# Optimization experiments

Hardware: AMD Instinct MI355X
Metric: run time of the kernel (lower is better)

The kernel has to match this reference:

```python
import jax, jax.numpy as jnp
import numpy as np

B, H, W, C, NH = 400, 14, 14, 768, 12
HD = C // NH  # 64


def setup_inputs() -> dict:
    key = jax.random.key(0)
    ks = jax.random.split(key, 6)
    s = 0.02
    return {
        "hidden_states": jax.random.normal(ks[0], (B, H, W, C), jnp.float32),
        "qkv_w": jax.random.normal(ks[1], (3 * C, C), jnp.float32) * s,
        "qkv_b": jnp.zeros((3 * C,), jnp.float32),
        "proj_w": jax.random.normal(ks[2], (C, C), jnp.float32) * s,
        "proj_b": jnp.zeros((C,), jnp.float32),
        "rel_pos_h": jax.random.normal(ks[3], (2 * H - 1, HD), jnp.float32) * s,
        "rel_pos_w": jax.random.normal(ks[4], (2 * W - 1, HD), jnp.float32) * s,
    }


def _get_rel_pos(q_size, k_size, rel_pos):
    # q_size == k_size and table already has 2*k-1 entries -> pure gather,
    # matching SamVisionAttention.get_rel_pos without interpolation.
    coords = jnp.arange(q_size)[:, None] - jnp.arange(k_size)[None, :] + (k_size - 1)
    return rel_pos[coords]  # (q, k, head_dim)


def reference(hidden_states, qkv_w, qkv_b, proj_w, proj_b, rel_pos_h, rel_pos_w):
    b, h, w, c = hidden_states.shape
    scale = HD ** -0.5
    # qkv projection: (b, h*w, 3c) -> (3, b, nh, hw, hd)
    qkv = hidden_states.reshape(b, h * w, c) @ qkv_w.T + qkv_b
    qkv = qkv.reshape(b, h * w, 3, NH, HD).transpose(2, 0, 3, 1, 4)
    q, k, v = qkv[0], qkv[1], qkv[2]
    # decomposed relative position bias (computed from UNSCALED q, as in SAM)
    Rh = _get_rel_pos(h, h, rel_pos_h)  # (h, h, hd)
    Rw = _get_rel_pos(w, w, rel_pos_w)  # (w, w, hd)
    qr = q.reshape(b, NH, h, w, HD)
    rel_h = jnp.einsum('bnhwc,hkc->bnhwk', qr, Rh)  # (b, nh, h, w, h)
    rel_w = jnp.einsum('bnhwc,wkc->bnhwk', qr, Rw)  # (b, nh, h, w, w)
    bias = (rel_h[..., :, None] + rel_w[..., None, :]).reshape(b, NH, h * w, h * w)
    # attention
    attn = jnp.einsum('bnqd,bnkd->bnqk', q, k) * scale + bias
    attn = jax.nn.softmax(attn, axis=-1)
    out = jnp.einsum('bnqk,bnkd->bnqd', attn, v)
    out = out.transpose(0, 2, 1, 3).reshape(b, h, w, c)
    return out @ proj_w.T + proj_b
```

## Files before the change

kernel.cpp:

```cpp
#include <hip/hip_runtime.h>
#include <hip/hip_bf16.h>

typedef __bf16 bfv8 __attribute__((ext_vector_type(8)));
typedef float f32x4 __attribute__((ext_vector_type(4)));
typedef unsigned short u16;
typedef unsigned int u32;

#define MT 78400

#define SBAR() __builtin_amdgcn_s_barrier()
#define VMCNT(n) asm volatile("s_waitcnt vmcnt(" #n ")" ::: "memory")

__device__ __forceinline__ u16 f2bf(float f) {
  u32 x = __float_as_uint(f);
  return (u16)((x + 0x7FFFu + ((x >> 16) & 1u)) >> 16);
}

__device__ __forceinline__ void gld16(const void* g, void* l) {
  __builtin_amdgcn_global_load_lds((const __attribute__((address_space(1))) void*)g,
                                   (__attribute__((address_space(3))) void*)l, 16, 0, 0);
}

__global__ __launch_bounds__(256) void cvt_f32_bf16(const float* __restrict__ src,
                                                    u16* __restrict__ dst, int n8) {
  int stride = gridDim.x * 256;
  for (int i = blockIdx.x * 256 + threadIdx.x; i < n8; i += stride) {
    const float4* s = (const float4*)(src + (long)i * 8);
    float4 a = s[0], b = s[1];
    u32 p0 = f2bf(a.x) | ((u32)f2bf(a.y) << 16);
    u32 p1 = f2bf(a.z) | ((u32)f2bf(a.w) << 16);
    u32 p2 = f2bf(b.x) | ((u32)f2bf(b.y) << 16);
    u32 p3 = f2bf(b.z) | ((u32)f2bf(b.w) << 16);
    uint4 o = {p0, p1, p2, p3};
    *(uint4*)(dst + (long)i * 8) = o;
  }
}


__device__ __forceinline__ void gemm256_main(const u16* __restrict__ A, const u16* __restrict__ W,
                                             u16* SH, int m0, int n0, int tid,
                                             f32x4 (&acc)[8][4]) {
  const int lane = tid & 63;
  const int q15 = lane & 15, g = lane >> 4;
  const int wid = tid >> 6;
  const int wm = wid >> 2, wn = wid & 3;
  const int x0 = (g ^ (q15 & 7)) << 3;
  const int arow0 = wm * 128 + q15;
  const int brow0 = wn * 64 + q15;

  const int r0 = tid >> 3;
  const int gc0 = ((tid & 7) ^ (r0 & 7)) << 3;
  int ra00 = m0 + r0;       if (ra00 > MT - 1) ra00 = MT - 1;
  int ra10 = m0 + 64 + r0;  if (ra10 > MT - 1) ra10 = MT - 1;
  int ra01 = m0 + 128 + r0; if (ra01 > MT - 1) ra01 = MT - 1;
  int ra11 = m0 + 192 + r0; if (ra11 > MT - 1) ra11 = MT - 1;
  const u16* aS00 = A + (long)ra00 * 768 + gc0;
  const u16* aS10 = A + (long)ra10 * 768 + gc0;
  const u16* aS01 = A + (long)ra01 * 768 + gc0;
  const u16* aS11 = A + (long)ra11 * 768 + gc0;
  const u16* bS00 = W + (long)(n0 + r0) * 768 + gc0;
  const u16* bS10 = W + (long)(n0 + 64 + r0) * 768 + gc0;
  const u16* bS01 = W + (long)(n0 + 128 + r0) * 768 + gc0;
  const u16* bS11 = W + (long)(n0 + 192 + r0) * 768 + gc0;
  u16* dA = SH + tid * 8;
  u16* dB = dA + 16384;

  auto STGA = [&](int sl, const u16* p0, const u16* p1, int hoff, int kt) {
    u16* d = dA + sl * 32768 + hoff;
    gld16(p0 + kt * 64, d);
    gld16(p1 + kt * 64, d + 4096);
  };
  auto STGB = [&](int sl, const u16* p0, const u16* p1, int hoff, int kt) {
    u16* d = dB + sl * 32768 + hoff;
    gld16(p0 + kt * 64, d);
    gld16(p1 + kt * 64, d + 4096);
  };

  bfv8 b0[4], b1[4];
  bfv8 aX0[2], aX1[2], aY0[2], aY1[2];

  STGB(0, bS00, bS10, 0, 0); STGB(0, bS01, bS11, 8192, 0);
  STGA(0, aS00, aS10, 0, 0); STGA(0, aS01, aS11, 8192, 0);
  STGB(1, bS00, bS10, 0, 1); STGB(1, bS01, bS11, 8192, 1);
  STGA(1, aS00, aS10, 0, 1);
  VMCNT(4);
  SBAR();
  {
    const u16* Sb = SH + 16384;
#pragma unroll
    for (int ni = 0; ni < 4; ++ni) {
      const u16* bp = Sb + (brow0 + ni * 16) * 64;
      b0[ni] = *(const bfv8*)(bp + x0);
      b1[ni] = *(const bfv8*)(bp + (x0 ^ 32));
    }
#pragma unroll
    for (int m2 = 0; m2 < 2; ++m2) {
      const u16* ap = SH + (arow0 + m2 * 16) * 64;
      aX0[m2] = *(const bfv8*)(ap + x0);
      aX1[m2] = *(const bfv8*)(ap + (x0 ^ 32));
    }
  }

  for (int u = 0; u < 12; ++u) {
    const int sl = u & 1;
    const u16* Sa = SH + sl * 32768;
    const u16* San = SH + (sl ^ 1) * 32768;
    const u16* Sbn = San + 16384;
    const int kn1 = (u + 1 < 12) ? u + 1 : 11;
    const int kn2 = (u + 2 < 12) ? u + 2 : 11;

    __builtin_amdgcn_s_setprio(1);
#pragma unroll
    for (int m2 = 0; m2 < 2; ++m2)
#pragma unroll
      for (int ni = 0; ni < 4; ++ni)
        acc[m2][ni] = __builtin_amdgcn_mfma_f32_16x16x32_bf16(aX0[m2], b0[ni], acc[m2][ni], 0, 0, 0);
#pragma unroll
    for (int m2 = 0; m2 < 2; ++m2)
#pragma unroll
      for (int ni = 0; ni < 4; ++ni)
        acc[m2][ni] = __builtin_amdgcn_mfma_f32_16x16x32_bf16(aX1[m2], b1[ni], acc[m2][ni], 0, 0, 0);
    __builtin_amdgcn_s_setprio(0);
    SBAR();
#pragma unroll
    for (int m2 = 0; m2 < 2; ++m2) {
      const u16* ap = Sa + (arow0 + (2 + m2) * 16) * 64;
      aY0[m2] = *(const bfv8*)(ap + x0);
      aY1[m2] = *(const bfv8*)(ap + (x0 ^ 32));
    }
    STGA(sl ^ 1, aS01, aS11, 8192, kn1);

    __builtin_amdgcn_s_setprio(1);
#pragma unroll
    for (int m2 = 0; m2 < 2; ++m2)
#pragma unroll
      for (int ni = 0; ni < 4; ++ni)
        acc[2 + m2][ni] = __builtin_amdgcn_mfma_f32_16x16x32_bf16(aY0[m2], b0[ni], acc[2 + m2][ni], 0, 0, 0);
#pragma unroll
    for (int m2 = 0; m2 < 2; ++m2)
#pragma unroll
      for (int ni = 0; ni < 4; ++ni)
        acc[2 + m2][ni] = __builtin_amdgcn_mfma_f32_16x16x32_bf16(aY1[m2], b1[ni], acc[2 + m2][ni], 0, 0, 0);
    __builtin_amdgcn_s_setprio(0);
    SBAR();
#pragma unroll
    for (int m2 = 0; m2 < 2; ++m2) {
      const u16* ap = Sa + (arow0 + (4 + m2) * 16) * 64;
      aX0[m2] = *(const bfv8*)(ap + x0);
      aX1[m2] = *(const bfv8*)(ap + (x0 ^ 32));
    }
    STGB(sl, bS00, bS10, 0, kn2);

    __builtin_amdgcn_s_setprio(1);
#pragma unroll
    for (int m2 = 0; m2 < 2; ++m2)
#pragma unroll
      for (int ni = 0; ni < 4; ++ni)
        acc[4 + m2][ni] = __builtin_amdgcn_mfma_f32_16x16x32_bf16(aX0[m2], b0[ni], acc[4 + m2][ni], 0, 0, 0);
#pragma unroll
    for (int m2 = 0; m2 < 2; ++m2)
#pragma unroll
      for (int ni = 0; ni < 4; ++ni)
        acc[4 + m2][ni] = __builtin_amdgcn_mfma_f32_16x16x32_bf16(aX1[m2], b1[ni], acc[4 + m2][ni], 0, 0, 0);
    __builtin_amdgcn_s_setprio(0);
    SBAR();
#pragma unroll
    for (int m2 = 0; m2 < 2; ++m2) {
      const u16* ap = Sa + (arow0 + (6 + m2) * 16) * 64;
      aY0[m2] = *(const bfv8*)(ap + x0);
      aY1[m2] = *(const bfv8*)(ap + (x0 ^ 32));
    }
    STGB(sl, bS01, bS11, 8192, kn2);

    __builtin_amdgcn_s_setprio(1);
#pragma unroll
    for (int m2 = 0; m2 < 2; ++m2)
#pragma unroll
      for (int ni = 0; ni < 4; ++ni)
        acc[6 + m2][ni] = __builtin_amdgcn_mfma_f32_16x16x32_bf16(aY0[m2], b0[ni], acc[6 + m2][ni], 0, 0, 0);
#pragma unroll
    for (int m2 = 0; m2 < 2; ++m2)
#pragma unroll
      for (int ni = 0; ni < 4; ++ni)
        acc[6 + m2][ni] = __builtin_amdgcn_mfma_f32_16x16x32_bf16(aY1[m2], b1[ni], acc[6 + m2][ni], 0, 0, 0);
    __builtin_amdgcn_s_setprio(0);
    VMCNT(4);
    SBAR();
    if (u < 11) {
#pragma unroll
      for (int ni = 0; ni < 4; ++ni) {
        const u16* bp = Sbn + (brow0 + ni * 16) * 64;
        b0[ni] = *(const bfv8*)(bp + x0);
        b1[ni] = *(const bfv8*)(bp + (x0 ^ 32));
      }
#pragma unroll
      for (int m2 = 0; m2 < 2; ++m2) {
        const u16* ap = San + (arow0 + m2 * 16) * 64;
        aX0[m2] = *(const bfv8*)(ap + x0);
        aX1[m2] = *(const bfv8*)(ap + (x0 ^ 32));
      }
    }
    STGA(sl, aS00, aS10, 0, kn2);
  }
  VMCNT(0);
}

__global__ __launch_bounds__(512, 2) void qkv_gemm(const u16* __restrict__ A, const u16* __restrict__ W,
                                                   const float* __restrict__ bias,
                                                   u16* __restrict__ Qo, u16* __restrict__ Ko,
                                                   u16* __restrict__ Vo) {
  extern __shared__ u16 SH[];
  const int tid = threadIdx.x;
  const int orig = blockIdx.x;
  const int xcd = orig & 7, ii = orig >> 3;
  const int wg = (xcd < 3 ? xcd * 346 : 1038 + (xcd - 3) * 345) + ii;
  const int mt = wg / 9, nt = wg - mt * 9;
  const int m0 = mt * 256, n0 = nt * 256;

  f32x4 acc[8][4];
#pragma unroll
  for (int i = 0; i < 8; ++i)
#pragma unroll
    for (int j = 0; j < 4; ++j) acc[i][j] = (f32x4){0.f, 0.f, 0.f, 0.f};

  gemm256_main(A, W, SH, m0, n0, tid, acc);

  const int lane = tid & 63, q15 = lane & 15, g = lane >> 4;
  const int wid = tid >> 6, wm = wid >> 2, wn = wid & 3;
  __syncthreads();
  const int sel = nt / 3;
  u16* dst = (sel == 0) ? Qo : (sel == 1) ? Ko : Vo;
  const int ntr = nt - sel * 3;
  u16* Cs = SH;

#pragma unroll
  for (int h = 0; h < 2; ++h) {
    if (wm == h) {
#pragma unroll
      for (int ni = 0; ni < 4; ++ni) {
        int col = wn * 64 + ni * 16 + q15;
        float bb = bias[n0 + col];
#pragma unroll
        for (int mi = 0; mi < 8; ++mi)
#pragma unroll
          for (int r = 0; r < 4; ++r)
            Cs[(mi * 16 + g * 4 + r) * 264 + col] = f2bf(acc[mi][ni][r] + bb);
      }
    }
    __syncthreads();
#pragma unroll
    for (int j = 0; j < 8; ++j) {
      int idx = tid + 512 * j;
      int row = idx >> 5, cc = idx & 31;
      int m = m0 + h * 128 + row;
      if (m < MT) {
        int b = m / 196, s = m - b * 196;
        int nh = ntr * 4 + (cc >> 3);
        int hd0 = (cc & 7) * 8;
        uint4 v = *(const uint4*)(Cs + row * 264 + cc * 8);
        *(uint4*)(dst + (long)b * 150528 + (long)s * 64 + nh * 12544 + hd0) = v;
      }
    }
    if (h == 0) __syncthreads();
  }
}

__global__ __launch_bounds__(512, 2) void proj_gemm(const u16* __restrict__ A, const u16* __restrict__ W,
                                                    const float* __restrict__ bias,
                                                    float* __restrict__ out) {
  extern __shared__ u16 SH[];
  const int tid = threadIdx.x;
  const int orig = blockIdx.x;
  const int xcd = orig & 7, ii = orig >> 3;
  const int wg = (xcd < 1 ? xcd * 116 : 116 + (xcd - 1) * 115) + ii;
  const int mt = wg / 3, nt = wg - mt * 3;
  const int m0 = mt * 256, n0 = nt * 256;

  f32x4 acc[8][4];
#pragma unroll
  for (int i = 0; i < 8; ++i)
#pragma unroll
    for (int j = 0; j < 4; ++j) acc[i][j] = (f32x4){0.f, 0.f, 0.f, 0.f};

  gemm256_main(A, W, SH, m0, n0, tid, acc);

  const int lane = tid & 63, q15 = lane & 15, g = lane >> 4;
  const int wid = tid >> 6, wm = wid >> 2, wn = wid & 3;

#pragma unroll
  for (int ni = 0; ni < 4; ++ni) {
    int n = n0 + wn * 64 + ni * 16 + q15;
    float bb = bias[n];
#pragma unroll
    for (int mi = 0; mi < 8; ++mi)
#pragma unroll
      for (int r = 0; r < 4; ++r) {
        int m = m0 + wm * 128 + mi * 16 + g * 4 + r;
        if (m < MT) out[(long)m * 768 + n] = acc[mi][ni][r] + bb;
      }
  }
}

#define KLDS_OFF 0
#define INDK_OFF 26624
#define VT_OFF   43264
#define TH_OFF   76032
#define TW_OFF   79920
#define AW_OFF   83808
#define P_OFF    94048
#define SMEM_SZ  153440

__global__ __launch_bounds__(512, 2) void attn_kernel(const u16* __restrict__ Q, const u16* __restrict__ K,
                                                      const u16* __restrict__ V,
                                                      const float* __restrict__ rph, const float* __restrict__ rpw,
                                                      u16* __restrict__ AO) {
  extern __shared__ char smem[];
  u16* Klds = (u16*)(smem + KLDS_OFF);
  u16* IndK = (u16*)(smem + INDK_OFF);
  u16* VT = (u16*)(smem + VT_OFF);
  u16* TH = (u16*)(smem + TH_OFF);
  u16* TW = (u16*)(smem + TW_OFF);
  const int tid = threadIdx.x, lane = tid & 63, wid = tid >> 6;
  const int q15 = lane & 15, g = lane >> 4;
  const int bnh = blockIdx.x;
  const int b = bnh / 12, nh = bnh - b * 12;
  const u16* Qg = Q + bnh * 12544;
  const u16* Kg = K + bnh * 12544;
  const u16* Vg = V + bnh * 12544;
  u16* Pw = (u16*)(smem + P_OFF) + wid * 16 * 232;
  u16* AWw = (u16*)(smem + AW_OFF) + wid * 16 * 40;

  for (int c = tid; c < 1568; c += 512) {
    int krow = c >> 3, part = c & 7;
    gld16(Kg + krow * 64 + ((part ^ (krow & 7)) << 3), Klds + c * 8);
  }
  for (int i = tid; i < 208 * 40; i += 512) {
    int k = i / 40, j = i - (i / 40) * 40;
    int hk = k / 14, wk = k - hk * 14;
    IndK[i] = (j == hk || j == 16 + wk) ? 0x3F80 : 0;
  }
  for (int idx = tid; idx < 1792; idx += 512) {
    int k = idx >> 3, nb = idx & 7;
    u32 w0 = 0, w1 = 0, w2 = 0, w3 = 0;
    if (k < 196) {
      uint4 t = *(const uint4*)(Vg + k * 64 + nb * 8);
      w0 = t.x; w1 = t.y; w2 = t.z; w3 = t.w;
    }
    u32 wv[4] = {w0, w1, w2, w3};
#pragma unroll
    for (int j = 0; j < 8; j++) {
      int n = nb * 8 + j;
      u16 val = (u16)(wv[j >> 1] >> ((j & 1) * 16));
      int blk = (k >> 3) ^ (n & 7) ^ (n >> 3);
      VT[n * 256 + blk * 8 + (k & 7)] = val;
    }
  }
  for (int i = tid; i < 27 * 64; i += 512) {
    int r = i >> 6, cc = i & 63;
    TH[r * 72 + cc] = f2bf(rph[i]);
    TW[r * 72 + cc] = f2bf(rpw[i]);
  }
  for (int i = lane; i < 16 * 24; i += 64) Pw[(i / 24) * 232 + 208 + (i % 24)] = 0;
  __syncthreads();

  const int ksw = q15 & 7;
  const int ko0 = (g ^ ksw) << 3;
  const int ko1 = ((g + 4) ^ ksw) << 3;

  const f32x4 zero = {0.f, 0.f, 0.f, 0.f};
  for (int qt = wid; qt < 13; qt += 8) {
    const int q0 = qt * 16;
    int qrow = q0 + q15; if (qrow > 195) qrow = 195;
    bfv8 qf0 = *(const bfv8*)(Qg + qrow * 64 + g * 8);
    bfv8 qf1 = *(const bfv8*)(Qg + qrow * 64 + 32 + g * 8);

    int hq0 = q0 / 14, hq1 = (q0 + 15) / 14;
    int rha = hq0 + 13 - q15; rha = rha < 0 ? 0 : (rha > 26 ? 26 : rha);
    int rhb = hq1 + 13 - q15; rhb = rhb < 0 ? 0 : (rhb > 26 ? 26 : rhb);
    int rwa = q15;
    int rwb = 16 + q15; if (rwb > 26) rwb = 26;
    f32x4 c0h = zero, c1h = zero, c0w = zero, c1w = zero;
    {
      bfv8 t0 = *(const bfv8*)(TH + rha * 72 + g * 8);
      bfv8 t1 = *(const bfv8*)(TH + rha * 72 + 32 + g * 8);
      c0h = __builtin_amdgcn_mfma_f32_16x16x32_bf16(qf0, t0, c0h, 0, 0, 0);
      c0h = __builtin_amdgcn_mfma_f32_16x16x32_bf16(qf1, t1, c0h, 0, 0, 0);
      bfv8 t2 = *(const bfv8*)(TH + rhb * 72 + g * 8);
      bfv8 t3 = *(const bfv8*)(TH + rhb * 72 + 32 + g * 8);
      c1h = __builtin_amdgcn_mfma_f32_16x16x32_bf16(qf0, t2, c1h, 0, 0, 0);
      c1h = __builtin_amdgcn_mfma_f32_16x16x32_bf16(qf1, t3, c1h, 0, 0, 0);
      bfv8 u0 = *(const bfv8*)(TW + rwa * 72 + g * 8);
      bfv8 u1 = *(const bfv8*)(TW + rwa * 72 + 32 + g * 8);
      c0w = __builtin_amdgcn_mfma_f32_16x16x32_bf16(qf0, u0, c0w, 0, 0, 0);
      c0w = __builtin_amdgcn_mfma_f32_16x16x32_bf16(qf1, u1, c0w, 0, 0, 0);
      bfv8 u2 = *(const bfv8*)(TW + rwb * 72 + g * 8);
      bfv8 u3 = *(const bfv8*)(TW + rwb * 72 + 32 + g * 8);
      c0w = c0w;
      c1w = __builtin_amdgcn_mfma_f32_16x16x32_bf16(qf0, u2, c1w, 0, 0, 0);
      c1w = __builtin_amdgcn_mfma_f32_16x16x32_bf16(qf1, u3, c1w, 0, 0, 0);
    }

#pragma unroll
    for (int r = 0; r < 4; r++) {
      int row = g * 4 + r;
      int qq = q0 + row;
      int hqr = qq / 14;
      int wq_r = qq - hqr * 14;
      if (q15 < 10) AWw[row * 40 + 30 + q15] = 0;
      float rh = ((hqr == hq1) ? c1h[r] : c0h[r]) * 8.0f;
      AWw[row * 40 + q15] = (q15 <= 13) ? f2bf(rh) : (u16)0;
      int w0p = wq_r + 13 - q15;
      if (w0p >= 0 && w0p <= 13) AWw[row * 40 + 16 + w0p] = f2bf(c0w[r] * 8.0f);
      int w1p = wq_r - 3 - q15;
      if (w1p >= 0 && w1p <= 13) AWw[row * 40 + 16 + w1p] = f2bf(c1w[r] * 8.0f);
    }
    bfv8 qaug = *(const bfv8*)(AWw + q15 * 40 + g * 8);

    float den = 0.f;
#pragma unroll
    for (int t = 0; t < 13; t++) {
      const u16* kr = Klds + (t * 16 + q15) * 64;
      bfv8 kb0 = *(const bfv8*)(kr + ko0);
      bfv8 kb1 = *(const bfv8*)(kr + ko1);
      bfv8 ib = *(const bfv8*)(IndK + (t * 16 + q15) * 40 + g * 8);
      __builtin_amdgcn_s_setprio(1);
      f32x4 a0 = __builtin_amdgcn_mfma_f32_16x16x32_bf16(ib, qaug, zero, 0, 0, 0);
      f32x4 a1 = __builtin_amdgcn_mfma_f32_16x16x32_bf16(kb0, qf0, a0, 0, 0, 0);
      f32x4 st = __builtin_amdgcn_mfma_f32_16x16x32_bf16(kb1, qf1, a1, 0, 0, 0);
      __builtin_amdgcn_s_setprio(0);
      float p0 = (t == 12 && g > 0) ? 0.f : exp2f(st[0] * 0.18033688f - 5.7707802f);
      float p1 = (t == 12 && g > 0) ? 0.f : exp2f(st[1] * 0.18033688f - 5.7707802f);
      float p2 = (t == 12 && g > 0) ? 0.f : exp2f(st[2] * 0.18033688f - 5.7707802f);
      float p3 = (t == 12 && g > 0) ? 0.f : exp2f(st[3] * 0.18033688f - 5.7707802f);
      den += (p0 + p1) + (p2 + p3);
      u32 lo, hi;
      asm("v_cvt_pk_bf16_f32 %0, %1, %2" : "=v"(lo) : "v"(p0), "v"(p1));
      asm("v_cvt_pk_bf16_f32 %0, %1, %2" : "=v"(hi) : "v"(p2), "v"(p3));
      uint2 pk = {lo, hi};
      *(uint2*)(Pw + q15 * 232 + t * 16 + g * 4) = pk;
    }
    den += __shfl_xor(den, 16);
    den += __shfl_xor(den, 32);
    float inv = 1.0f / den;
    float invr[4];
#pragma unroll
    for (int r = 0; r < 4; r++) invr[r] = __shfl(inv, g * 4 + r);

    f32x4 o[4] = {zero, zero, zero, zero};
    __builtin_amdgcn_s_setprio(1);
#pragma unroll
    for (int ks = 0; ks < 7; ks++) {
      bfv8 pa = *(const bfv8*)(Pw + q15 * 232 + ks * 32 + g * 8);
#pragma unroll
      for (int nt = 0; nt < 4; nt++) {
        int n = nt * 16 + q15;
        int blk = ((ks * 4 + g) ^ (n & 7) ^ (n >> 3));
        bfv8 vb = *(const bfv8*)(VT + n * 256 + blk * 8);
        o[nt] = __builtin_amdgcn_mfma_f32_16x16x32_bf16(pa, vb, o[nt], 0, 0, 0);
      }
    }
    __builtin_amdgcn_s_setprio(0);

#pragma unroll
    for (int nt = 0; nt < 4; nt++)
#pragma unroll
      for (int r = 0; r < 4; r++) {
        int s_ = q0 + g * 4 + r;
        if (s_ < 196) AO[((long)(b * 196 + s_)) * 768 + nh * 64 + nt * 16 + q15] = f2bf(o[nt][r] * invr[r]);
      }
  }
}

#define GEMM_LDS 131072

extern "C" void kernel_launch(void* const* d_in, const int* in_sizes, int n_in,
                              void* d_out, int out_size, void* d_ws, size_t ws_size,
                              hipStream_t stream) {
  const float* hs = (const float*)d_in[0];
  const float* qkvw = (const float*)d_in[1];
  const float* qkvb = (const float*)d_in[2];
  const float* projw = (const float*)d_in[3];
  const float* projb = (const float*)d_in[4];
  const float* rph = (const float*)d_in[5];
  const float* rpw = (const float*)d_in[6];

  char* ws = (char*)d_ws;
  u16* Xb = (u16*)ws;
  u16* Wq = (u16*)(ws + 120422400);
  u16* Wp = (u16*)(ws + 123961344);
  u16* Qb = (u16*)(ws + 125140992);
  u16* Kb = (u16*)(ws + 245563392);
  u16* Vb = (u16*)(ws + 365985792);
  u16* AO = Xb;

  cvt_f32_bf16<<<2048, 256, 0, stream>>>(hs, Xb, 7526400);
  cvt_f32_bf16<<<864, 256, 0, stream>>>(qkvw, Wq, 221184);
  cvt_f32_bf16<<<288, 256, 0, stream>>>(projw, Wp, 73728);

  hipFuncSetAttribute((const void*)qkv_gemm, hipFuncAttributeMaxDynamicSharedMemorySize, GEMM_LDS);
  qkv_gemm<<<2763, 512, GEMM_LDS, stream>>>(Xb, Wq, qkvb, Qb, Kb, Vb);

  hipFuncSetAttribute((const void*)attn_kernel, hipFuncAttributeMaxDynamicSharedMemorySize, SMEM_SZ);
  attn_kernel<<<4800, 512, SMEM_SZ, stream>>>(Qb, Kb, Vb, rph, rpw, AO);

  hipFuncSetAttribute((const void*)proj_gemm, hipFuncAttributeMaxDynamicSharedMemorySize, GEMM_LDS);
  proj_gemm<<<921, 512, GEMM_LDS, stream>>>(AO, Wp, projb, (float*)d_out);
}
```

Measured before the change: 821.5 us.

## Keep softmax probabilities in registers and shrink attention LDS for higher occupancy

The attention kernel no longer writes the P matrix to shared memory. It keeps the packed bf16 probabilities in registers and feeds them straight into 16x16x16 MFMAs, relying on the S accumulator layout matching the A-operand layout. The indicator matrix IndK now comes from global memory, filled by a small init kernel into the reused Wq buffer after the QKV GEMM. LDS drops from about 150KB to 77KB and launch bounds rise to 4 blocks per CU; the costs are more registers, more PV instructions at half K depth, and global or cache loads for IndK inside the inner loop.

```diff
diff --git a/kernel.cpp b/kernel.cpp
--- a/kernel.cpp
+++ b/kernel.cpp
@@ -2,7 +2,9 @@
 #include <hip/hip_bf16.h>
 
 typedef __bf16 bfv8 __attribute__((ext_vector_type(8)));
+typedef __bf16 bfv4 __attribute__((ext_vector_type(4)));
 typedef float f32x4 __attribute__((ext_vector_type(4)));
+typedef unsigned int u32x2 __attribute__((ext_vector_type(2)));
 typedef unsigned short u16;
 typedef unsigned int u32;
 
@@ -36,6 +38,14 @@
   }
 }
 
+__global__ __launch_bounds__(256) void indk_init(u16* __restrict__ T) {
+  int i = blockIdx.x * 256 + threadIdx.x;
+  if (i < 208 * 40) {
+    int k = i / 40, j = i - (i / 40) * 40;
+    int hk = k / 14, wk = k - hk * 14;
+    T[i] = (j == hk || j == 16 + wk) ? 0x3F80 : 0;
+  }
+}
 
 __device__ __forceinline__ void gemm256_main(const u16* __restrict__ A, const u16* __restrict__ W,
                                              u16* SH, int m0, int n0, int tid,
@@ -302,21 +312,19 @@
 }
 
 #define KLDS_OFF 0
-#define INDK_OFF 26624
-#define VT_OFF   43264
-#define TH_OFF   76032
-#define TW_OFF   79920
-#define AW_OFF   83808
-#define P_OFF    94048
-#define SMEM_SZ  153440
-
-__global__ __launch_bounds__(512, 2) void attn_kernel(const u16* __restrict__ Q, const u16* __restrict__ K,
+#define VT_OFF   26624
+#define TH_OFF   59392
+#define TW_OFF   63280
+#define AW_OFF   67168
+#define SMEM_SZ  77408
+
+__global__ __launch_bounds__(512, 4) void attn_kernel(const u16* __restrict__ Q, const u16* __restrict__ K,
                                                       const u16* __restrict__ V,
                                                       const float* __restrict__ rph, const float* __restrict__ rpw,
+                                                      const u16* __restrict__ IndKg,
                                                       u16* __restrict__ AO) {
   extern __shared__ char smem[];
   u16* Klds = (u16*)(smem + KLDS_OFF);
-  u16* IndK = (u16*)(smem + INDK_OFF);
   u16* VT = (u16*)(smem + VT_OFF);
   u16* TH = (u16*)(smem + TH_OFF);
   u16* TW = (u16*)(smem + TW_OFF);
@@ -327,17 +335,11 @@
   const u16* Qg = Q + bnh * 12544;
   const u16* Kg = K + bnh * 12544;
   const u16* Vg = V + bnh * 12544;
-  u16* Pw = (u16*)(smem + P_OFF) + wid * 16 * 232;
   u16* AWw = (u16*)(smem + AW_OFF) + wid * 16 * 40;
 
   for (int c = tid; c < 1568; c += 512) {
     int krow = c >> 3, part = c & 7;
     gld16(Kg + krow * 64 + ((part ^ (krow & 7)) << 3), Klds + c * 8);
-  }
-  for (int i = tid; i < 208 * 40; i += 512) {
-    int k = i / 40, j = i - (i / 40) * 40;
-    int hk = k / 14, wk = k - hk * 14;
-    IndK[i] = (j == hk || j == 16 + wk) ? 0x3F80 : 0;
   }
   for (int idx = tid; idx < 1792; idx += 512) {
     int k = idx >> 3, nb = idx & 7;
@@ -360,7 +362,6 @@
     TH[r * 72 + cc] = f2bf(rph[i]);
     TW[r * 72 + cc] = f2bf(rpw[i]);
   }
-  for (int i = lane; i < 16 * 24; i += 64) Pw[(i / 24) * 232 + 208 + (i % 24)] = 0;
   __syncthreads();
 
   const int ksw = q15 & 7;
@@ -395,7 +396,6 @@
       c0w = __builtin_amdgcn_mfma_f32_16x16x32_bf16(qf1, u1, c0w, 0, 0, 0);
       bfv8 u2 = *(const bfv8*)(TW + rwb * 72 + g * 8);
       bfv8 u3 = *(const bfv8*)(TW + rwb * 72 + 32 + g * 8);
-      c0w = c0w;
       c1w = __builtin_amdgcn_mfma_f32_16x16x32_bf16(qf0, u2, c1w, 0, 0, 0);
       c1w = __builtin_amdgcn_mfma_f32_16x16x32_bf16(qf1, u3, c1w, 0, 0, 0);
     }
@@ -416,13 +416,14 @@
     }
     bfv8 qaug = *(const bfv8*)(AWw + q15 * 40 + g * 8);
 
+    u32 pkA[13], pkB[13];
     float den = 0.f;
 #pragma unroll
     for (int t = 0; t < 13; t++) {
       const u16* kr = Klds + (t * 16 + q15) * 64;
       bfv8 kb0 = *(const bfv8*)(kr + ko0);
       bfv8 kb1 = *(const bfv8*)(kr + ko1);
-      bfv8 ib = *(const bfv8*)(IndK + (t * 16 + q15) * 40 + g * 8);
+      bfv8 ib = *(const bfv8*)(IndKg + (t * 16 + q15) * 40 + g * 8);
       __builtin_amdgcn_s_setprio(1);
       f32x4 a0 = __builtin_amdgcn_mfma_f32_16x16x32_bf16(ib, qaug, zero, 0, 0, 0);
       f32x4 a1 = __builtin_amdgcn_mfma_f32_16x16x32_bf16(kb0, qf0, a0, 0, 0, 0);
@@ -436,8 +437,7 @@
       u32 lo, hi;
       asm("v_cvt_pk_bf16_f32 %0, %1, %2" : "=v"(lo) : "v"(p0), "v"(p1));
       asm("v_cvt_pk_bf16_f32 %0, %1, %2" : "=v"(hi) : "v"(p2), "v"(p3));
-      uint2 pk = {lo, hi};
-      *(uint2*)(Pw + q15 * 232 + t * 16 + g * 4) = pk;
+      pkA[t] = lo; pkB[t] = hi;
     }
     den += __shfl_xor(den, 16);
     den += __shfl_xor(den, 32);
@@ -449,24 +449,27 @@
     f32x4 o[4] = {zero, zero, zero, zero};
     __builtin_amdgcn_s_setprio(1);
 #pragma unroll
-    for (int ks = 0; ks < 7; ks++) {
-      bfv8 pa = *(const bfv8*)(Pw + q15 * 232 + ks * 32 + g * 8);
-#pragma unroll
-      for (int nt = 0; nt < 4; nt++) {
-        int n = nt * 16 + q15;
-        int blk = ((ks * 4 + g) ^ (n & 7) ^ (n >> 3));
-        bfv8 vb = *(const bfv8*)(VT + n * 256 + blk * 8);
-        o[nt] = __builtin_amdgcn_mfma_f32_16x16x32_bf16(pa, vb, o[nt], 0, 0, 0);
+    for (int t = 0; t < 13; t++) {
+      u32x2 w; w.x = pkA[t]; w.y = pkB[t];
+      bfv4 pa = __builtin_bit_cast(bfv4, w);
+      const int kblk = 2 * t + (g >> 1);
+      const int koff = (g & 1) * 4;
+#pragma unroll
+      for (int nt_ = 0; nt_ < 4; nt_++) {
+        int n = nt_ * 16 + q15;
+        int blk = (kblk ^ (n & 7) ^ (n >> 3));
+        bfv4 vb = *(const bfv4*)(VT + n * 256 + blk * 8 + koff);
+        asm("v_mfma_f32_16x16x16_bf16 %0, %1, %2, %0" : "+v"(o[nt_]) : "v"(pa), "v"(vb));
       }
     }
     __builtin_amdgcn_s_setprio(0);
 
 #pragma unroll
-    for (int nt = 0; nt < 4; nt++)
+    for (int nt_ = 0; nt_ < 4; nt_++)
 #pragma unroll
       for (int r = 0; r < 4; r++) {
         int s_ = q0 + g * 4 + r;
-        if (s_ < 196) AO[((long)(b * 196 + s_)) * 768 + nh * 64 + nt * 16 + q15] = f2bf(o[nt][r] * invr[r]);
+        if (s_ < 196) AO[((long)(b * 196 + s_)) * 768 + nh * 64 + nt_ * 16 + q15] = f2bf(o[nt_][r] * invr[r]);
       }
   }
 }
@@ -492,6 +495,7 @@
   u16* Kb = (u16*)(ws + 245563392);
   u16* Vb = (u16*)(ws + 365985792);
   u16* AO = Xb;
+  u16* IndKg = Wq;
 
   cvt_f32_bf16<<<2048, 256, 0, stream>>>(hs, Xb, 7526400);
   cvt_f32_bf16<<<864, 256, 0, stream>>>(qkvw, Wq, 221184);
@@ -500,8 +504,10 @@
   hipFuncSetAttribute((const void*)qkv_gemm, hipFuncAttributeMaxDynamicSharedMemorySize, GEMM_LDS);
   qkv_gemm<<<2763, 512, GEMM_LDS, stream>>>(Xb, Wq, qkvb, Qb, Kb, Vb);
 
+  indk_init<<<33, 256, 0, stream>>>(IndKg);
+
   hipFuncSetAttribute((const void*)attn_kernel, hipFuncAttributeMaxDynamicSharedMemorySize, SMEM_SZ);
-  attn_kernel<<<4800, 512, SMEM_SZ, stream>>>(Qb, Kb, Vb, rph, rpw, AO);
+  attn_kernel<<<4800, 512, SMEM_SZ, stream>>>(Qb, Kb, Vb, rph, rpw, IndKg, AO);
 
   hipFuncSetAttribute((const void*)proj_gemm, hipFuncAttributeMaxDynamicSharedMemorySize, GEMM_LDS);
   proj_gemm<<<921, 512, GEMM_LDS, stream>>>(AO, Wp, projb, (float*)d_out);
```

Measured after the change: 1.005 ms. 1.22x slower.
